# Kernel optimization log

Measured on AMD Instinct MI355X. Metric: run time of the kernel, lower is better.

## Reference

```python
import jax, jax.numpy as jnp
import numpy as np

D_MODEL = 1024
N_HEADS = 16
HIDDEN = int(D_MODEL * 4 * 2 / 3)  # 2730, matches torch int(d*4*2/3)
EPS = 1e-6


def setup_inputs() -> dict:
    key = jax.random.key(0)
    ks = jax.random.split(key, 8)
    B, T = 4, 2048
    s = 0.02
    return {
        "x": jax.random.normal(ks[0], (B, T, D_MODEL), dtype=jnp.float32),
        "w_attn": jax.random.normal(ks[1], (D_MODEL, 3 * D_MODEL), dtype=jnp.float32) * s,
        "w_proj": jax.random.normal(ks[2], (D_MODEL, D_MODEL), dtype=jnp.float32) * s,
        "w1": jax.random.normal(ks[3], (D_MODEL, HIDDEN), dtype=jnp.float32) * s,
        "w2": jax.random.normal(ks[4], (D_MODEL, HIDDEN), dtype=jnp.float32) * s,
        "w3": jax.random.normal(ks[5], (HIDDEN, D_MODEL), dtype=jnp.float32) * s,
        "g1": jnp.ones((D_MODEL,), dtype=jnp.float32),
        "g2": jnp.ones((D_MODEL,), dtype=jnp.float32),
    }


def rmsnorm(x, g):
    norm = jax.lax.rsqrt(jnp.mean(x * x, axis=-1, keepdims=True) + EPS)
    return x * norm * g


def reference(x, w_attn, w_proj, w1, w2, w3, g1, g2):
    B, T, C = x.shape
    H = N_HEADS
    hd = C // H

    # attention branch
    qkv = rmsnorm(x, g1) @ w_attn                     # [B,T,3C]
    q, k, v = jnp.split(qkv, 3, axis=-1)
    q = q.reshape(B, T, H, hd).transpose(0, 2, 1, 3)  # [B,H,T,hd]
    k = k.reshape(B, T, H, hd).transpose(0, 2, 1, 3)
    v = v.reshape(B, T, H, hd).transpose(0, 2, 1, 3)

    att = jnp.einsum("bhqd,bhkd->bhqk", q, k) / jnp.sqrt(jnp.float32(hd))
    causal = jnp.tril(jnp.ones((T, T), dtype=bool))
    att = jnp.where(causal[None, None], att, jnp.float32(-jnp.inf))
    att = jax.nn.softmax(att, axis=-1)
    y = jnp.einsum("bhqk,bhkd->bhqd", att, v)          # [B,H,T,hd]
    y = y.transpose(0, 2, 1, 3).reshape(B, T, C)
    attn_out = y @ w_proj

    # parallel MLP branch on ln_2(x) (note: applied to x, not x+attn)
    h = rmsnorm(x, g2)
    mlp_out = (jax.nn.silu(h @ w1) * (h @ w2)) @ w3

    # dropout is identity in eval mode
    return x + attn_out + mlp_out
```

## Files before the change

kernel.cpp:

```cpp
#include <hip/hip_runtime.h>

#define TT 2048
#define DM 1024
#define HPAD 2816
#define HID 2730

typedef __attribute__((ext_vector_type(4))) float f32x4;
typedef __attribute__((ext_vector_type(8))) short bf16x8;

static __device__ __forceinline__ float bf2f(short u) {
    union { float f; unsigned int i; } c; c.i = ((unsigned int)(unsigned short)u) << 16; return c.f;
}
static __device__ __forceinline__ short f2bf(float f) {
    union { float f; unsigned int i; } c; c.f = f;
    unsigned int i = c.i;
    unsigned int r = (i + 0x7fffu + ((i >> 16) & 1u)) >> 16;
    return (short)r;
}

static __device__ __forceinline__ void gload_lds16(const void* g, void* l) {
    __builtin_amdgcn_global_load_lds(
        (const __attribute__((address_space(1))) unsigned int*)g,
        (__attribute__((address_space(3))) unsigned int*)l, 16, 0, 0);
}

__global__ __launch_bounds__(256) void wprep(const float* __restrict__ in, short* __restrict__ out,
                                             int K, int N, int Kpad, int Npad) {
    __shared__ float tile[32][33];
    int kb = blockIdx.x * 32, nb = blockIdx.y * 32;
    int tx = threadIdx.x, ty = threadIdx.y;
    #pragma unroll
    for (int i = 0; i < 32; i += 8) {
        int k = kb + ty + i, n = nb + tx;
        float v = (k < K && n < N) ? in[(size_t)k * N + n] : 0.f;
        tile[tx][ty + i] = v;
    }
    __syncthreads();
    #pragma unroll
    for (int i = 0; i < 32; i += 8) {
        int n = nb + ty + i, k = kb + tx;
        if (n < Npad && k < Kpad) out[(size_t)n * Kpad + k] = f2bf(tile[ty + i][tx]);
    }
}

__global__ __launch_bounds__(256) void rmsnorm2(const float* __restrict__ x,
    const float* __restrict__ g1, const float* __restrict__ g2,
    short* __restrict__ xn1, short* __restrict__ xn2) {
    int row = blockIdx.x;
    const float* xr = x + (size_t)row * DM;
    int t = threadIdx.x;
    float4 v = ((const float4*)xr)[t];
    float ss = v.x*v.x + v.y*v.y + v.z*v.z + v.w*v.w;
    #pragma unroll
    for (int off = 1; off < 64; off <<= 1) ss += __shfl_xor(ss, off);
    __shared__ float red[4];
    if ((t & 63) == 0) red[t >> 6] = ss;
    __syncthreads();
    float tot = red[0] + red[1] + red[2] + red[3];
    float rs = rsqrtf(tot * (1.0f / DM) + 1e-6f);
    float4 G1 = ((const float4*)g1)[t];
    float4 G2 = ((const float4*)g2)[t];
    union { short s[4]; int2 v; } o1, o2;
    o1.s[0] = f2bf(v.x * rs * G1.x); o1.s[1] = f2bf(v.y * rs * G1.y);
    o1.s[2] = f2bf(v.z * rs * G1.z); o1.s[3] = f2bf(v.w * rs * G1.w);
    o2.s[0] = f2bf(v.x * rs * G2.x); o2.s[1] = f2bf(v.y * rs * G2.y);
    o2.s[2] = f2bf(v.z * rs * G2.z); o2.s[3] = f2bf(v.w * rs * G2.w);
    *(int2*)(xn1 + (size_t)row * DM + t * 4) = o1.v;
    *(int2*)(xn2 + (size_t)row * DM + t * 4) = o2.v;
}

template<int EPI>
__global__ __launch_bounds__(256) void gemm_bt(
    const short* __restrict__ A, const short* __restrict__ Bt,
    short* __restrict__ Cb, const float* __restrict__ X, float* __restrict__ Of,
    int M, int N, int K)
{
    __shared__ short As[128 * 64];
    __shared__ short Bs[128 * 64];
    int t = threadIdx.x;
    int wid = t >> 6, l = t & 63;
    int wm = wid >> 1, wn = wid & 1;

    int nwg = gridDim.x, bid = blockIdx.x;
    int wg = (bid & 7) * (nwg >> 3) + (bid >> 3);
    int tiles_n = N >> 7;
    int tm = wg / tiles_n, tn = wg % tiles_n;

    const short* Arow = A + (size_t)(tm * 128) * K;
    const short* Brow = Bt + (size_t)(tn * 128) * K;

    f32x4 acc[4][4];
    #pragma unroll
    for (int m = 0; m < 4; m++)
        #pragma unroll
        for (int n = 0; n < 4; n++) acc[m][n] = (f32x4){0.f, 0.f, 0.f, 0.f};

    for (int kt = 0; kt < K; kt += 64) {
        __syncthreads();
        #pragma unroll
        for (int i = 0; i < 4; i++) {
            int linear = i * 256 + t;
            int row = linear >> 3;
            int slot = linear & 7;
            int srcslot = slot ^ (row & 7);
            gload_lds16(Arow + (size_t)row * K + kt + srcslot * 8, (char*)As + linear * 16);
            gload_lds16(Brow + (size_t)row * K + kt + srcslot * 8, (char*)Bs + linear * 16);
        }
        __syncthreads();
        #pragma unroll
        for (int ks = 0; ks < 2; ks++) {
            bf16x8 af[4], bfr[4];
            #pragma unroll
            for (int m = 0; m < 4; m++) {
                int row = wm * 64 + m * 16 + (l & 15);
                af[m] = *(const bf16x8*)((char*)As + row * 128 + ((ks * 64 + (l >> 4) * 16) ^ ((row & 7) << 4)));
            }
            #pragma unroll
            for (int n = 0; n < 4; n++) {
                int row = wn * 64 + n * 16 + (l & 15);
                bfr[n] = *(const bf16x8*)((char*)Bs + row * 128 + ((ks * 64 + (l >> 4) * 16) ^ ((row & 7) << 4)));
            }
            #pragma unroll
            for (int m = 0; m < 4; m++)
                #pragma unroll
                for (int n = 0; n < 4; n++)
                    acc[m][n] = __builtin_amdgcn_mfma_f32_16x16x32_bf16(af[m], bfr[n], acc[m][n], 0, 0, 0);
        }
    }

    #pragma unroll
    for (int m = 0; m < 4; m++)
        #pragma unroll
        for (int n = 0; n < 4; n++)
            #pragma unroll
            for (int r = 0; r < 4; r++) {
                int row = tm * 128 + wm * 64 + m * 16 + (l >> 4) * 4 + r;
                int col = tn * 128 + wn * 64 + n * 16 + (l & 15);
                size_t idx = (size_t)row * N + col;
                float v = acc[m][n][r];
                if constexpr (EPI == 0) Cb[idx] = f2bf(v);
                else if constexpr (EPI == 1) Of[idx] = X[idx] + v;
                else if constexpr (EPI == 4) Of[idx] += v;
            }
}

__global__ __launch_bounds__(512, 2) void gemm_mlp2(
    const short* __restrict__ A, const short* __restrict__ B1t, const short* __restrict__ B2t,
    short* __restrict__ Cb, int M, int N, int K)
{
    __shared__ short As[128 * 64];
    __shared__ short B1s[128 * 64];
    __shared__ short B2s[128 * 64];
    int t = threadIdx.x;
    int wid = t >> 6, l = t & 63;
    int wm = wid >> 2, wn = wid & 3;

    int nwg = gridDim.x, bid = blockIdx.x;
    int wg = (bid & 7) * (nwg >> 3) + (bid >> 3);
    int tiles_n = N >> 7;
    int tm = wg / tiles_n, tn = wg % tiles_n;

    const short* Arow  = A   + (size_t)(tm * 128) * K;
    const short* B1row = B1t + (size_t)(tn * 128) * K;
    const short* B2row = B2t + (size_t)(tn * 128) * K;

    f32x4 acc1[4][2], acc2[4][2];
    #pragma unroll
    for (int m = 0; m < 4; m++)
        #pragma unroll
        for (int n = 0; n < 2; n++) {
            acc1[m][n] = (f32x4){0.f, 0.f, 0.f, 0.f};
            acc2[m][n] = (f32x4){0.f, 0.f, 0.f, 0.f};
        }

    for (int kt = 0; kt < K; kt += 64) {
        __syncthreads();
        #pragma unroll
        for (int i = 0; i < 2; i++) {
            int linear = i * 512 + t;
            int row = linear >> 3;
            int slot = linear & 7;
            int srcslot = slot ^ (row & 7);
            gload_lds16(Arow  + (size_t)row * K + kt + srcslot * 8, (char*)As  + linear * 16);
            gload_lds16(B1row + (size_t)row * K + kt + srcslot * 8, (char*)B1s + linear * 16);
            gload_lds16(B2row + (size_t)row * K + kt + srcslot * 8, (char*)B2s + linear * 16);
        }
        __syncthreads();
        #pragma unroll
        for (int ks = 0; ks < 2; ks++) {
            bf16x8 af[4], b1[2], b2[2];
            #pragma unroll
            for (int m = 0; m < 4; m++) {
                int row = wm * 64 + m * 16 + (l & 15);
                int off = (ks * 64 + (l >> 4) * 16) ^ ((row & 7) << 4);
                af[m] = *(const bf16x8*)((char*)As + row * 128 + off);
            }
            #pragma unroll
            for (int n = 0; n < 2; n++) {
                int row = wn * 32 + n * 16 + (l & 15);
                int off = (ks * 64 + (l >> 4) * 16) ^ ((row & 7) << 4);
                b1[n] = *(const bf16x8*)((char*)B1s + row * 128 + off);
                b2[n] = *(const bf16x8*)((char*)B2s + row * 128 + off);
            }
            #pragma unroll
            for (int m = 0; m < 4; m++)
                #pragma unroll
                for (int n = 0; n < 2; n++) {
                    acc1[m][n] = __builtin_amdgcn_mfma_f32_16x16x32_bf16(af[m], b1[n], acc1[m][n], 0, 0, 0);
                    acc2[m][n] = __builtin_amdgcn_mfma_f32_16x16x32_bf16(af[m], b2[n], acc2[m][n], 0, 0, 0);
                }
        }
    }

    #pragma unroll
    for (int m = 0; m < 4; m++)
        #pragma unroll
        for (int n = 0; n < 2; n++)
            #pragma unroll
            for (int r = 0; r < 4; r++) {
                int row = tm * 128 + wm * 64 + m * 16 + (l >> 4) * 4 + r;
                int col = tn * 128 + wn * 32 + n * 16 + (l & 15);
                float v1 = acc1[m][n][r];
                float v2 = acc2[m][n][r];
                Cb[(size_t)row * N + col] = f2bf(v1 * (1.f / (1.f + __expf(-v1))) * v2);
            }
}

#define PSTR 76
#define SM_C 0.18033688f
__global__ __launch_bounds__(512, 4) void attn(const short* __restrict__ qkv, short* __restrict__ y) {
    __shared__ short Ks[2][64 * 64];
    __shared__ short Vt[2][64 * 64];
    __shared__ short Ps[8][16 * PSTR];
    int bid = blockIdx.x;
    int xcd = bid & 7;
    int idx = bid >> 3;
    int bh  = xcd + 8 * (idx >> 3);
    int pair = idx & 7;
    int b = bh >> 4, h = bh & 15;
    int t = threadIdx.x, wid = t >> 6, l = t & 63;
    const size_t base = (size_t)b * TT * 3072;

    int krow = t >> 3, kslot = t & 7, ksrc = kslot ^ (krow & 7);
    int vrow = t >> 3, vch = t & 7;

    #pragma unroll
    for (int pass = 0; pass < 2; pass++) {
        int qt = pass == 0 ? (15 - pair) : pair;
        int q0 = qt * 128 + wid * 16;

        bf16x8 qf[2];
        #pragma unroll
        for (int s = 0; s < 2; s++) {
            int row = q0 + (l & 15);
            qf[s] = *(const bf16x8*)(qkv + base + (size_t)row * 3072 + h * 64 + s * 32 + (l >> 4) * 8);
        }

        f32x4 o[4];
        #pragma unroll
        for (int n = 0; n < 4; n++) o[n] = (f32x4){0.f, 0.f, 0.f, 0.f};
        float ll[4];
        #pragma unroll
        for (int r = 0; r < 4; r++) ll[r] = 0.f;

        int nt = 2 * qt + 2;

        {
            gload_lds16(qkv + base + (size_t)krow * 3072 + 1024 + h * 64 + ksrc * 8,
                        (char*)Ks + t * 16);
            uint4 vv = *(const uint4*)(qkv + base + (size_t)vrow * 3072 + 2048 + h * 64 + vch * 8);
            const short* vs = (const short*)&vv;
            #pragma unroll
            for (int j = 0; j < 8; j++) {
                int d = vch * 8 + j;
                int byte = (d * 128 + vrow * 2) ^ (((j ^ vch) & 7) << 4);
                *(short*)((char*)Vt + byte) = vs[j];
            }
            __syncthreads();
        }

        int cur = 0;
        for (int it = 0; it < nt; ++it) {
            int kb = it << 6;
            bool have_next = (it + 1 < nt);
            uint4 vv;
            if (have_next) {
                int nkb = kb + 64;
                gload_lds16(qkv + base + (size_t)(nkb + krow) * 3072 + 1024 + h * 64 + ksrc * 8,
                            (char*)Ks + (cur ^ 1) * 8192 + t * 16);
                vv = *(const uint4*)(qkv + base + (size_t)(nkb + vrow) * 3072 + 2048 + h * 64 + vch * 8);
            }
            if (kb <= q0 + 15) {
                f32x4 s4[4];
                __builtin_amdgcn_s_setprio(1);
                #pragma unroll
                for (int j = 0; j < 4; j++) {
                    f32x4 z = (f32x4){0.f, 0.f, 0.f, 0.f};
                    #pragma unroll
                    for (int ks = 0; ks < 2; ks++) {
                        int row = j * 16 + (l & 15);
                        bf16x8 kf = *(const bf16x8*)((char*)Ks + cur * 8192 + row * 128 +
                                    ((ks * 64 + (l >> 4) * 16) ^ ((row & 7) << 4)));
                        z = __builtin_amdgcn_mfma_f32_16x16x32_bf16(qf[ks], kf, z, 0, 0, 0);
                    }
                    s4[j] = z;
                }
                __builtin_amdgcn_s_setprio(0);
                bool diag = (kb + 63 > q0);
                #pragma unroll
                for (int j = 0; j < 4; j++)
                    #pragma unroll
                    for (int r = 0; r < 4; r++) {
                        float v = s4[j][r];
                        if (diag) {
                            int qrow = q0 + (l >> 4) * 4 + r;
                            int kcol = kb + j * 16 + (l & 15);
                            if (kcol > qrow) v = -3e38f;
                        }
                        float p = exp2f(v * SM_C);
                        s4[j][r] = p;
                        ll[r] += p;
                    }

                short* P = &Ps[wid][0];
                #pragma unroll
                for (int j = 0; j < 4; j++)
                    #pragma unroll
                    for (int r = 0; r < 4; r++)
                        P[((l >> 4) * 4 + r) * PSTR + j * 16 + (l & 15)] = f2bf(s4[j][r]);

                bf16x8 pf[2];
                #pragma unroll
                for (int ks = 0; ks < 2; ks++)
                    pf[ks] = *(const bf16x8*)(P + (l & 15) * PSTR + ks * 32 + (l >> 4) * 8);
                __builtin_amdgcn_s_setprio(1);
                #pragma unroll
                for (int n = 0; n < 4; n++) {
                    #pragma unroll
                    for (int ks = 0; ks < 2; ks++) {
                        int vr = n * 16 + (l & 15);
                        int f = (vr & 7) ^ ((vr >> 3) & 7);
                        bf16x8 vf = *(const bf16x8*)((char*)Vt + cur * 8192 + vr * 128 +
                                    ((ks * 64 + (l >> 4) * 16) ^ (f << 4)));
                        o[n] = __builtin_amdgcn_mfma_f32_16x16x32_bf16(pf[ks], vf, o[n], 0, 0, 0);
                    }
                }
                __builtin_amdgcn_s_setprio(0);
            }
            if (have_next) {
                const short* vs = (const short*)&vv;
                #pragma unroll
                for (int j = 0; j < 8; j++) {
                    int d = vch * 8 + j;
                    int byte = (d * 128 + vrow * 2) ^ (((j ^ vch) & 7) << 4);
                    *(short*)((char*)Vt + (cur ^ 1) * 8192 + byte) = vs[j];
                }
            }
            __syncthreads();
            cur ^= 1;
        }

        #pragma unroll
        for (int r = 0; r < 4; r++) {
            #pragma unroll
            for (int off = 1; off < 16; off <<= 1) ll[r] += __shfl_xor(ll[r], off);
        }
        float inv[4];
        #pragma unroll
        for (int r = 0; r < 4; r++) inv[r] = 1.f / ll[r];
        #pragma unroll
        for (int n = 0; n < 4; n++)
            #pragma unroll
            for (int r = 0; r < 4; r++) {
                int row = q0 + (l >> 4) * 4 + r;
                int col = h * 64 + n * 16 + (l & 15);
                y[(size_t)(b * TT + row) * DM + col] = f2bf(o[n][r] * inv[r]);
            }
    }
}

extern "C" void kernel_launch(void* const* d_in, const int* in_sizes, int n_in,
                              void* d_out, int out_size, void* d_ws, size_t ws_size,
                              hipStream_t stream) {
    (void)in_sizes; (void)n_in; (void)out_size; (void)ws_size;
    const float* x      = (const float*)d_in[0];
    const float* w_attn = (const float*)d_in[1];
    const float* w_proj = (const float*)d_in[2];
    const float* w1     = (const float*)d_in[3];
    const float* w2     = (const float*)d_in[4];
    const float* w3     = (const float*)d_in[5];
    const float* g1     = (const float*)d_in[6];
    const float* g2     = (const float*)d_in[7];
    float* out = (float*)d_out;

    char* ws = (char*)d_ws;
    size_t off = 0;
    auto alloc = [&](size_t bytes) { char* p = ws + off; off += (bytes + 255) & ~(size_t)255; return p; };
    short* wattn_t = (short*)alloc((size_t)3072 * 1024 * 2);
    short* wproj_t = (short*)alloc((size_t)1024 * 1024 * 2);
    short* w1t     = (short*)alloc((size_t)HPAD * 1024 * 2);
    short* w2t     = (short*)alloc((size_t)HPAD * 1024 * 2);
    short* w3t     = (short*)alloc((size_t)1024 * HPAD * 2);
    short* xn1     = (short*)alloc((size_t)8192 * 1024 * 2);
    short* xn2     = (short*)alloc((size_t)8192 * 1024 * 2);
    short* qkvb    = (short*)alloc((size_t)8192 * 3072 * 2);
    short* yb      = (short*)alloc((size_t)8192 * 1024 * 2);
    short* hb      = (short*)alloc((size_t)8192 * HPAD * 2);

    dim3 tb(32, 8);
    wprep<<<dim3(32, 96), tb, 0, stream>>>(w_attn, wattn_t, 1024, 3072, 1024, 3072);
    wprep<<<dim3(32, 32), tb, 0, stream>>>(w_proj, wproj_t, 1024, 1024, 1024, 1024);
    wprep<<<dim3(32, 88), tb, 0, stream>>>(w1, w1t, 1024, HID, 1024, HPAD);
    wprep<<<dim3(32, 88), tb, 0, stream>>>(w2, w2t, 1024, HID, 1024, HPAD);
    wprep<<<dim3(88, 32), tb, 0, stream>>>(w3, w3t, HID, 1024, HPAD, 1024);

    rmsnorm2<<<8192, 256, 0, stream>>>(x, g1, g2, xn1, xn2);

    gemm_bt<0><<<1536, 256, 0, stream>>>(xn1, wattn_t, qkvb, nullptr, nullptr, 8192, 3072, 1024);
    attn<<<512, 512, 0, stream>>>(qkvb, yb);
    gemm_bt<1><<<512, 256, 0, stream>>>(yb, wproj_t, nullptr, x, out, 8192, 1024, 1024);
    gemm_mlp2<<<1408, 512, 0, stream>>>(xn2, w1t, w2t, hb, 8192, HPAD, 1024);
    gemm_bt<4><<<512, 256, 0, stream>>>(hb, w3t, nullptr, nullptr, out, 8192, 1024, HPAD);
}
```

Measured before the change: 384.0 us.

## Fuse proj and w3 GEMMs, use 256-row tiles, keep attention P in registers

The GEMM now uses 256x128 tiles with 512 threads. The attention-projection and MLP down-projection GEMMs are merged into one kernel that walks both K ranges into a shared accumulator, so the output is no longer read-modify-written twice. The QKV GEMM folds the softmax scale into the Q columns. The attention kernel computes S transposed so P can be packed to bf16 and moved between lanes with shuffles instead of a shared-memory round trip, and the row-sum reduction is simplified. The larger tiles and the fused launch reduce grid size and may lower occupancy, and the QK^T bf16 truncation now drops bits rather than rounding.

```diff
diff --git a/kernel.cpp b/kernel.cpp
--- a/kernel.cpp
+++ b/kernel.cpp
@@ -4,6 +4,7 @@
 #define DM 1024
 #define HPAD 2816
 #define HID 2730
+#define SM_C 0.18033688f
 
 typedef __attribute__((ext_vector_type(4))) float f32x4;
 typedef __attribute__((ext_vector_type(8))) short bf16x8;
@@ -16,6 +17,10 @@
     unsigned int i = c.i;
     unsigned int r = (i + 0x7fffu + ((i >> 16) & 1u)) >> 16;
     return (short)r;
+}
+static __device__ __forceinline__ unsigned int fbits(float f) {
+    union { float f; unsigned int i; } c; c.f = f;
+    return c.i;
 }
 
 static __device__ __forceinline__ void gload_lds16(const void* g, void* l) {
@@ -70,12 +75,13 @@
 }
 
 template<int EPI>
-__global__ __launch_bounds__(256) void gemm_bt(
+__global__ __launch_bounds__(512, 4) void gemm256(
     const short* __restrict__ A, const short* __restrict__ Bt,
+    const short* __restrict__ A2, const short* __restrict__ B2,
     short* __restrict__ Cb, const float* __restrict__ X, float* __restrict__ Of,
-    int M, int N, int K)
+    int N, int K1, int K2)
 {
-    __shared__ short As[128 * 64];
+    __shared__ short As[256 * 64];
     __shared__ short Bs[128 * 64];
     int t = threadIdx.x;
     int wid = t >> 6, l = t & 63;
@@ -86,25 +92,39 @@
     int tiles_n = N >> 7;
     int tm = wg / tiles_n, tn = wg % tiles_n;
 
-    const short* Arow = A + (size_t)(tm * 128) * K;
-    const short* Brow = Bt + (size_t)(tn * 128) * K;
-
     f32x4 acc[4][4];
     #pragma unroll
     for (int m = 0; m < 4; m++)
         #pragma unroll
         for (int n = 0; n < 4; n++) acc[m][n] = (f32x4){0.f, 0.f, 0.f, 0.f};
 
-    for (int kt = 0; kt < K; kt += 64) {
+    int nt1 = K1 >> 6;
+    int NT = (EPI == 1) ? nt1 + (K2 >> 6) : nt1;
+
+    for (int kt = 0; kt < NT; ++kt) {
+        const short* Ab; const short* Bb; int K; int kk;
+        if constexpr (EPI == 1) {
+            if (kt < nt1) { Ab = A;  Bb = Bt; K = K1; kk = kt; }
+            else          { Ab = A2; Bb = B2; K = K2; kk = kt - nt1; }
+        } else { Ab = A; Bb = Bt; K = K1; kk = kt; }
+        const short* Arow = Ab + (size_t)(tm * 256) * K + kk * 64;
+        const short* Brow = Bb + (size_t)(tn * 128) * K + kk * 64;
         __syncthreads();
         #pragma unroll
         for (int i = 0; i < 4; i++) {
-            int linear = i * 256 + t;
-            int row = linear >> 3;
-            int slot = linear & 7;
-            int srcslot = slot ^ (row & 7);
-            gload_lds16(Arow + (size_t)row * K + kt + srcslot * 8, (char*)As + linear * 16);
-            gload_lds16(Brow + (size_t)row * K + kt + srcslot * 8, (char*)Bs + linear * 16);
+            int lin = i * 512 + t;
+            int row = lin >> 3;
+            int slot = lin & 7;
+            int src = slot ^ (row & 7);
+            gload_lds16(Arow + (size_t)row * K + src * 8, (char*)As + lin * 16);
+        }
+        #pragma unroll
+        for (int i = 0; i < 2; i++) {
+            int lin = i * 512 + t;
+            int row = lin >> 3;
+            int slot = lin & 7;
+            int src = slot ^ (row & 7);
+            gload_lds16(Brow + (size_t)row * K + src * 8, (char*)Bs + lin * 16);
         }
         __syncthreads();
         #pragma unroll
@@ -120,27 +140,30 @@
                 int row = wn * 64 + n * 16 + (l & 15);
                 bfr[n] = *(const bf16x8*)((char*)Bs + row * 128 + ((ks * 64 + (l >> 4) * 16) ^ ((row & 7) << 4)));
             }
+            __builtin_amdgcn_s_setprio(1);
             #pragma unroll
             for (int m = 0; m < 4; m++)
                 #pragma unroll
                 for (int n = 0; n < 4; n++)
                     acc[m][n] = __builtin_amdgcn_mfma_f32_16x16x32_bf16(af[m], bfr[n], acc[m][n], 0, 0, 0);
+            __builtin_amdgcn_s_setprio(0);
         }
     }
 
+    bool qcols = (EPI == 5) && (tn < 8);
     #pragma unroll
     for (int m = 0; m < 4; m++)
         #pragma unroll
         for (int n = 0; n < 4; n++)
             #pragma unroll
             for (int r = 0; r < 4; r++) {
-                int row = tm * 128 + wm * 64 + m * 16 + (l >> 4) * 4 + r;
+                int row = tm * 256 + wm * 64 + m * 16 + (l >> 4) * 4 + r;
                 int col = tn * 128 + wn * 64 + n * 16 + (l & 15);
                 size_t idx = (size_t)row * N + col;
                 float v = acc[m][n][r];
                 if constexpr (EPI == 0) Cb[idx] = f2bf(v);
+                else if constexpr (EPI == 5) Cb[idx] = f2bf(qcols ? v * SM_C : v);
                 else if constexpr (EPI == 1) Of[idx] = X[idx] + v;
-                else if constexpr (EPI == 4) Of[idx] += v;
             }
 }
 
@@ -226,12 +249,9 @@
             }
 }
 
-#define PSTR 76
-#define SM_C 0.18033688f
 __global__ __launch_bounds__(512, 4) void attn(const short* __restrict__ qkv, short* __restrict__ y) {
     __shared__ short Ks[2][64 * 64];
     __shared__ short Vt[2][64 * 64];
-    __shared__ short Ps[8][16 * PSTR];
     int bid = blockIdx.x;
     int xcd = bid & 7;
     int idx = bid >> 3;
@@ -248,6 +268,7 @@
     for (int pass = 0; pass < 2; pass++) {
         int qt = pass == 0 ? (15 - pair) : pair;
         int q0 = qt * 128 + wid * 16;
+        int qrow = q0 + (l & 15);
 
         bf16x8 qf[2];
         #pragma unroll
@@ -259,9 +280,7 @@
         f32x4 o[4];
         #pragma unroll
         for (int n = 0; n < 4; n++) o[n] = (f32x4){0.f, 0.f, 0.f, 0.f};
-        float ll[4];
-        #pragma unroll
-        for (int r = 0; r < 4; r++) ll[r] = 0.f;
+        float ll = 0.f;
 
         int nt = 2 * qt + 2;
 
@@ -291,7 +310,8 @@
                 vv = *(const uint4*)(qkv + base + (size_t)(nkb + vrow) * 3072 + 2048 + h * 64 + vch * 8);
             }
             if (kb <= q0 + 15) {
-                f32x4 s4[4];
+                bool diag = (kb + 63 > q0);
+                unsigned int pk[4][2];
                 __builtin_amdgcn_s_setprio(1);
                 #pragma unroll
                 for (int j = 0; j < 4; j++) {
@@ -301,51 +321,45 @@
                         int row = j * 16 + (l & 15);
                         bf16x8 kf = *(const bf16x8*)((char*)Ks + cur * 8192 + row * 128 +
                                     ((ks * 64 + (l >> 4) * 16) ^ ((row & 7) << 4)));
-                        z = __builtin_amdgcn_mfma_f32_16x16x32_bf16(qf[ks], kf, z, 0, 0, 0);
+                        z = __builtin_amdgcn_mfma_f32_16x16x32_bf16(kf, qf[ks], z, 0, 0, 0);
                     }
-                    s4[j] = z;
+                    float p[4];
+                    #pragma unroll
+                    for (int r = 0; r < 4; r++) {
+                        float v = z[r];
+                        if (diag) {
+                            int kcol = kb + j * 16 + (l >> 4) * 4 + r;
+                            if (kcol > qrow) v = -3e38f;
+                        }
+                        p[r] = exp2f(v);
+                        ll += p[r];
+                    }
+                    pk[j][0] = (fbits(p[1]) & 0xffff0000u) | (fbits(p[0]) >> 16);
+                    pk[j][1] = (fbits(p[3]) & 0xffff0000u) | (fbits(p[2]) >> 16);
                 }
                 __builtin_amdgcn_s_setprio(0);
-                bool diag = (kb + 63 > q0);
+
                 #pragma unroll
-                for (int j = 0; j < 4; j++)
+                for (int ks = 0; ks < 2; ks++) {
+                    union { unsigned int u[4]; bf16x8 v; } pa;
                     #pragma unroll
-                    for (int r = 0; r < 4; r++) {
-                        float v = s4[j][r];
-                        if (diag) {
-                            int qrow = q0 + (l >> 4) * 4 + r;
-                            int kcol = kb + j * 16 + (l & 15);
-                            if (kcol > qrow) v = -3e38f;
-                        }
-                        float p = exp2f(v * SM_C);
-                        s4[j][r] = p;
-                        ll[r] += p;
+                    for (int w = 0; w < 4; w++) {
+                        int src = (((l >> 4) & 1) << 5) | ((w >> 1) << 4) | (l & 15);
+                        unsigned int a = __shfl(pk[2 * ks][w & 1], src);
+                        unsigned int bb = __shfl(pk[2 * ks + 1][w & 1], src);
+                        pa.u[w] = (l >> 5) ? bb : a;
                     }
-
-                short* P = &Ps[wid][0];
-                #pragma unroll
-                for (int j = 0; j < 4; j++)
+                    __builtin_amdgcn_s_setprio(1);
                     #pragma unroll
-                    for (int r = 0; r < 4; r++)
-                        P[((l >> 4) * 4 + r) * PSTR + j * 16 + (l & 15)] = f2bf(s4[j][r]);
-
-                bf16x8 pf[2];
-                #pragma unroll
-                for (int ks = 0; ks < 2; ks++)
-                    pf[ks] = *(const bf16x8*)(P + (l & 15) * PSTR + ks * 32 + (l >> 4) * 8);
-                __builtin_amdgcn_s_setprio(1);
-                #pragma unroll
-                for (int n = 0; n < 4; n++) {
-                    #pragma unroll
-                    for (int ks = 0; ks < 2; ks++) {
+                    for (int n = 0; n < 4; n++) {
                         int vr = n * 16 + (l & 15);
                         int f = (vr & 7) ^ ((vr >> 3) & 7);
                         bf16x8 vf = *(const bf16x8*)((char*)Vt + cur * 8192 + vr * 128 +
                                     ((ks * 64 + (l >> 4) * 16) ^ (f << 4)));
-                        o[n] = __builtin_amdgcn_mfma_f32_16x16x32_bf16(pf[ks], vf, o[n], 0, 0, 0);
+                        o[n] = __builtin_amdgcn_mfma_f32_16x16x32_bf16(pa.v, vf, o[n], 0, 0, 0);
                     }
+                    __builtin_amdgcn_s_setprio(0);
                 }
-                __builtin_amdgcn_s_setprio(0);
             }
             if (have_next) {
                 const short* vs = (const short*)&vv;
@@ -360,22 +374,19 @@
             cur ^= 1;
         }
 
+        ll += __shfl_xor(ll, 16);
+        ll += __shfl_xor(ll, 32);
+        float inv = 1.f / ll;
         #pragma unroll
         for (int r = 0; r < 4; r++) {
-            #pragma unroll
-            for (int off = 1; off < 16; off <<= 1) ll[r] += __shfl_xor(ll[r], off);
-        }
-        float inv[4];
-        #pragma unroll
-        for (int r = 0; r < 4; r++) inv[r] = 1.f / ll[r];
-        #pragma unroll
-        for (int n = 0; n < 4; n++)
-            #pragma unroll
-            for (int r = 0; r < 4; r++) {
+            float invr = __shfl(inv, (l >> 4) * 4 + r);
+            #pragma unroll
+            for (int n = 0; n < 4; n++) {
                 int row = q0 + (l >> 4) * 4 + r;
                 int col = h * 64 + n * 16 + (l & 15);
-                y[(size_t)(b * TT + row) * DM + col] = f2bf(o[n][r] * inv[r]);
-            }
+                y[(size_t)(b * TT + row) * DM + col] = f2bf(o[n][r] * invr);
+            }
+        }
     }
 }
 
@@ -416,9 +427,10 @@
 
     rmsnorm2<<<8192, 256, 0, stream>>>(x, g1, g2, xn1, xn2);
 
-    gemm_bt<0><<<1536, 256, 0, stream>>>(xn1, wattn_t, qkvb, nullptr, nullptr, 8192, 3072, 1024);
+    gemm256<5><<<768, 512, 0, stream>>>(xn1, wattn_t, nullptr, nullptr,
+                                        qkvb, nullptr, nullptr, 3072, 1024, 0);
     attn<<<512, 512, 0, stream>>>(qkvb, yb);
-    gemm_bt<1><<<512, 256, 0, stream>>>(yb, wproj_t, nullptr, x, out, 8192, 1024, 1024);
     gemm_mlp2<<<1408, 512, 0, stream>>>(xn2, w1t, w2t, hb, 8192, HPAD, 1024);
-    gemm_bt<4><<<512, 256, 0, stream>>>(hb, w3t, nullptr, nullptr, out, 8192, 1024, HPAD);
-}
+    gemm256<1><<<256, 512, 0, stream>>>(yb, wproj_t, hb, w3t,
+                                        nullptr, x, out, 1024, 1024, HPAD);
+}
```

Measured after the change: 364.7 us. 5.0% less time.
